# Optimization experiments

Hardware: AMD Instinct MI355X
Metric: run time of the kernel (lower is better)

Reference implementation:

```python
import jax, jax.numpy as jnp
import numpy as np

N = 50000      # nodes
E = 800000     # edges (avg degree 16)
S = 2          # sample_size
D_IN = 128     # input_dim
D_NOISE = 64   # noise_dim
D0 = 256       # output_dims[0]
D1 = 256       # output_dims[1]


def setup_inputs() -> dict:
    key = jax.random.key(0)
    ks = jax.random.split(key, 8)
    X = jax.random.normal(ks[0], (1, N, D_IN), dtype=jnp.float32)
    edge_src = jax.random.randint(ks[1], (E,), 0, N)
    edge_dst = jax.random.randint(ks[2], (E,), 0, N)
    # Bernoulli(0.5) noise, as in torch.distributions.Bernoulli
    epsilon = (jax.random.uniform(ks[3], (S, N, D_NOISE)) < 0.5).astype(jnp.float32)
    W0 = jax.random.normal(ks[4], (D_IN + D_NOISE, D0), dtype=jnp.float32) * 0.05
    b0 = jnp.zeros((D0,), jnp.float32)
    W1 = jax.random.normal(ks[5], (D0, D1), dtype=jnp.float32) * 0.05
    b1 = jnp.zeros((D1,), jnp.float32)
    eps0 = jnp.zeros((), jnp.float32)  # GINConv learnable eps, init 0
    eps1 = jnp.zeros((), jnp.float32)
    return dict(X=X, epsilon=epsilon, edge_src=edge_src, edge_dst=edge_dst,
                W0=W0, b0=b0, W1=W1, b1=b1, eps0=eps0, eps1=eps1)


def reference(X, epsilon, edge_src, edge_dst, W0, b0, W1, b1, eps0, eps1):
    # Expand features over sample dim and concat noise: [S, N, D_IN + D_NOISE]
    feat = jnp.broadcast_to(X, (epsilon.shape[0], X.shape[1], X.shape[2]))
    h = jnp.concatenate([feat, epsilon], axis=2)

    def gin_layer(h, eps, W, b):
        # sum aggregation over in-edges: agg[:, d] += h[:, s] for each edge (s, d)
        agg = jnp.zeros_like(h).at[:, edge_dst, :].add(h[:, edge_src, :])
        return jax.nn.relu(((1.0 + eps) * h + agg) @ W + b)

    h = gin_layer(h, eps0, W0, b0)
    h = gin_layer(h, eps1, W1, b1)
    out = jax.nn.relu(h)  # outer activation applied once more in forward()
    return out, epsilon
```

## Files before the change

### kernel.cpp

```cpp
#include <hip/hip_runtime.h>
#include <hip/hip_bf16.h>

#define NN 50000
#define NE 800000
#define NS 2
#define DIN 128
#define DNOISE 64
#define DH0 192
#define DOUT 256
#define NB 49

typedef __bf16 bf16x8 __attribute__((ext_vector_type(8)));
typedef float floatx4 __attribute__((ext_vector_type(4)));


__device__ inline float bflo(unsigned int u) { return __uint_as_float(u << 16); }
__device__ inline float bfhi(unsigned int u) { return __uint_as_float(u & 0xffff0000u); }
__device__ inline unsigned short f2bf_bits(float x) {
    __hip_bfloat16 b = __float2bfloat16(x);
    return *reinterpret_cast<unsigned short*>(&b);
}
__device__ inline unsigned int pack2(float lo, float hi) {
    return (unsigned int)f2bf_bits(lo) | ((unsigned int)f2bf_bits(hi) << 16);
}


__global__ void count_kernel(const int* __restrict__ dst, int* __restrict__ cnt) {
    int i = blockIdx.x * blockDim.x + threadIdx.x;
    if (i < NE) atomicAdd(&cnt[dst[i]], 1);
}

__global__ __launch_bounds__(1024) void scanA_kernel(const int* __restrict__ cnt, int* __restrict__ bsum) {
    int i = blockIdx.x * 1024 + threadIdx.x;
    int v = (i < NN) ? cnt[i] : 0;
    for (int off = 32; off > 0; off >>= 1) v += __shfl_down(v, off);
    __shared__ int wsum[16];
    if ((threadIdx.x & 63) == 0) wsum[threadIdx.x >> 6] = v;
    __syncthreads();
    if (threadIdx.x == 0) {
        int s = 0;
        for (int k = 0; k < 16; ++k) s += wsum[k];
        bsum[blockIdx.x] = s;
    }
}

__global__ __launch_bounds__(64) void scanB_kernel(int* __restrict__ bsum) {
    int lane = threadIdx.x;
    int orig = (lane < NB) ? bsum[lane] : 0;
    int v = orig;
    for (int off = 1; off < 64; off <<= 1) {
        int t = __shfl_up(v, off);
        if (lane >= off) v += t;
    }
    if (lane < NB) bsum[lane] = v - orig;
}

__global__ __launch_bounds__(1024) void scanC_kernel(int* __restrict__ cnt, const int* __restrict__ bsum,
                                                     int* __restrict__ row_ptr) {
    __shared__ int buf[1024];
    int tid = threadIdx.x;
    int i = blockIdx.x * 1024 + tid;
    int v = (i < NN) ? cnt[i] : 0;
    buf[tid] = v;
    __syncthreads();
    for (int off = 1; off < 1024; off <<= 1) {
        int t = (tid >= off) ? buf[tid - off] : 0;
        __syncthreads();
        buf[tid] += t;
        __syncthreads();
    }
    int excl = buf[tid] - v + bsum[blockIdx.x];
    if (i < NN) { row_ptr[i + 1] = excl + v; cnt[i] = excl; }
    if (i == 0) row_ptr[0] = 0;
}

__global__ void fill_kernel(const int* __restrict__ src, const int* __restrict__ dst,
                            int* __restrict__ cursor, int* __restrict__ col_idx) {
    int i = blockIdx.x * blockDim.x + threadIdx.x;
    if (i < NE) {
        int p = atomicAdd(&cursor[dst[i]], 1);
        col_idx[p] = src[i];
    }
}

#define XQ (NN * DIN / 4)
#define XB4 ((XQ + 255) / 256)
#define NR_BLOCKS ((NS * NN + 255) / 256)

__global__ void prep_kernel(const float* __restrict__ X, unsigned short* __restrict__ Xb,
                            const float* __restrict__ noise, uint2* __restrict__ Nbit,
                            float* __restrict__ out_eps) {
    int b = blockIdx.x;
    if (b < XB4) {
        int i = b * 256 + threadIdx.x;
        if (i < XQ) {
            float4 v = reinterpret_cast<const float4*>(X)[i];
            ushort4 o;
            o.x = f2bf_bits(v.x); o.y = f2bf_bits(v.y); o.z = f2bf_bits(v.z); o.w = f2bf_bits(v.w);
            reinterpret_cast<ushort4*>(Xb)[i] = o;
        }
    } else {
        int r = (b - XB4) * 256 + threadIdx.x;
        if (r < NS * NN) {
            const float4* p = reinterpret_cast<const float4*>(noise + (size_t)r * DNOISE);
            float4* oe = reinterpret_cast<float4*>(out_eps + (size_t)r * DNOISE);
            unsigned int lo = 0, hi = 0;
            for (int q = 0; q < 8; ++q) {
                float4 v = p[q];
                oe[q] = v;
                int base = q * 4;
                lo |= (v.x != 0.f ? 1u : 0u) << base;
                lo |= (v.y != 0.f ? 1u : 0u) << (base + 1);
                lo |= (v.z != 0.f ? 1u : 0u) << (base + 2);
                lo |= (v.w != 0.f ? 1u : 0u) << (base + 3);
            }
            for (int q = 8; q < 16; ++q) {
                float4 v = p[q];
                oe[q] = v;
                int base = q * 4 - 32;
                hi |= (v.x != 0.f ? 1u : 0u) << base;
                hi |= (v.y != 0.f ? 1u : 0u) << (base + 1);
                hi |= (v.z != 0.f ? 1u : 0u) << (base + 2);
                hi |= (v.w != 0.f ? 1u : 0u) << (base + 3);
            }
            uint2 o; o.x = lo; o.y = hi;
            Nbit[r] = o;
        }
    }
}


__global__ void transpose_both(const float* __restrict__ W0, const float* __restrict__ W1,
                               __hip_bfloat16* __restrict__ Wt0, __hip_bfloat16* __restrict__ Wt1) {
    int b = blockIdx.x;
    if (b < DOUT) {
        for (int k = threadIdx.x; k < DH0; k += blockDim.x)
            Wt0[(size_t)b * DH0 + k] = __float2bfloat16(W0[(size_t)k * DOUT + b]);
    } else {
        int n = b - DOUT;
        for (int k = threadIdx.x; k < DOUT; k += blockDim.x)
            Wt1[(size_t)n * DOUT + k] = __float2bfloat16(W1[(size_t)k * DOUT + n]);
    }
}


__global__ __launch_bounds__(256) void agg0_kernel(
    const unsigned int* __restrict__ Xb,
    const uint2* __restrict__ Nbit,
    const int* __restrict__ row_ptr, const int* __restrict__ col_idx,
    const float* __restrict__ eps0p,
    unsigned int* __restrict__ z0) {
    const int d = blockIdx.x * 2 + (threadIdx.x >> 7);
    const int cc = threadIdx.x & 127;
    const float c = 1.f + eps0p[0];
    const int beg = row_ptr[d], end = row_ptr[d + 1];
    if (cc < 64) {
        const unsigned int* src = Xb + cc;
        unsigned int u = src[(size_t)d * 64];
        float aL = c * bflo(u), aH = c * bfhi(u);
        int e = beg;
        for (; e + 3 < end; e += 4) {
            int i0 = col_idx[e], i1 = col_idx[e + 1], i2 = col_idx[e + 2], i3 = col_idx[e + 3];
            unsigned int u0 = src[(size_t)i0 * 64], u1 = src[(size_t)i1 * 64];
            unsigned int u2 = src[(size_t)i2 * 64], u3 = src[(size_t)i3 * 64];
            aL += (bflo(u0) + bflo(u1)) + (bflo(u2) + bflo(u3));
            aH += (bfhi(u0) + bfhi(u1)) + (bfhi(u2) + bfhi(u3));
        }
        for (; e < end; ++e) {
            unsigned int ue = src[(size_t)col_idx[e] * 64];
            aL += bflo(ue); aH += bfhi(ue);
        }
        unsigned int r = pack2(aL, aH);
        z0[(size_t)d * 96 + cc] = r;
        z0[(size_t)(NN + d) * 96 + cc] = r;
    } else {
        int j = cc - 64;
        int s = j >> 5, col = j & 31;
        const uint2* src = Nbit + (size_t)s * NN;
        const int word = col >> 4;
        const int sh = (2 * col) & 31;
        uint2 uS = src[d];
        unsigned int wS = word ? uS.y : uS.x;
        int c0 = 0, c1 = 0;
        int e = beg;
        for (; e + 3 < end; e += 4) {
            uint2 u0 = src[col_idx[e]], u1 = src[col_idx[e + 1]];
            uint2 u2 = src[col_idx[e + 2]], u3 = src[col_idx[e + 3]];
            unsigned int w0 = word ? u0.y : u0.x, w1 = word ? u1.y : u1.x;
            unsigned int w2 = word ? u2.y : u2.x, w3 = word ? u3.y : u3.x;
            c0 += (int)((w0 >> sh) & 1) + (int)((w1 >> sh) & 1) + (int)((w2 >> sh) & 1) + (int)((w3 >> sh) & 1);
            c1 += (int)((w0 >> (sh + 1)) & 1) + (int)((w1 >> (sh + 1)) & 1) +
                  (int)((w2 >> (sh + 1)) & 1) + (int)((w3 >> (sh + 1)) & 1);
        }
        for (; e < end; ++e) {
            uint2 ue = src[col_idx[e]];
            unsigned int we = word ? ue.y : ue.x;
            c0 += (int)((we >> sh) & 1);
            c1 += (int)((we >> (sh + 1)) & 1);
        }
        float aL = c * (float)((wS >> sh) & 1) + (float)c0;
        float aH = c * (float)((wS >> (sh + 1)) & 1) + (float)c1;
        z0[(size_t)(s * NN + d) * 96 + 64 + col] = pack2(aL, aH);
    }
}


__global__ __launch_bounds__(128) void agg1_kernel(
    const uint2* __restrict__ h,
    const int* __restrict__ row_ptr, const int* __restrict__ col_idx,
    const float* __restrict__ eps1p,
    uint2* __restrict__ z1,
    int s) {
    const int d = blockIdx.x * 2 + (threadIdx.x >> 6);
    const int cc = threadIdx.x & 63;
    const float c = 1.f + eps1p[0];
    const int beg = row_ptr[d], end = row_ptr[d + 1];
    const uint2* src = h + (size_t)s * NN * 64 + cc;
    uint2 u = src[(size_t)d * 64];
    float aL0 = c * bflo(u.x), aH0 = c * bfhi(u.x);
    float aL1 = c * bflo(u.y), aH1 = c * bfhi(u.y);
    int e = beg;
    for (; e + 7 < end; e += 8) {
        uint2 g[8];
#pragma unroll
        for (int q = 0; q < 8; ++q) g[q] = src[(size_t)col_idx[e + q] * 64];
#pragma unroll
        for (int q = 0; q < 8; ++q) {
            aL0 += bflo(g[q].x); aH0 += bfhi(g[q].x);
            aL1 += bflo(g[q].y); aH1 += bfhi(g[q].y);
        }
    }
    for (; e + 3 < end; e += 4) {
        uint2 u0 = src[(size_t)col_idx[e] * 64], u1 = src[(size_t)col_idx[e + 1] * 64];
        uint2 u2 = src[(size_t)col_idx[e + 2] * 64], u3 = src[(size_t)col_idx[e + 3] * 64];
        aL0 += (bflo(u0.x) + bflo(u1.x)) + (bflo(u2.x) + bflo(u3.x));
        aH0 += (bfhi(u0.x) + bfhi(u1.x)) + (bfhi(u2.x) + bfhi(u3.x));
        aL1 += (bflo(u0.y) + bflo(u1.y)) + (bflo(u2.y) + bflo(u3.y));
        aH1 += (bfhi(u0.y) + bfhi(u1.y)) + (bfhi(u2.y) + bfhi(u3.y));
    }
    for (; e < end; ++e) {
        uint2 ue = src[(size_t)col_idx[e] * 64];
        aL0 += bflo(ue.x); aH0 += bfhi(ue.x);
        aL1 += bflo(ue.y); aH1 += bfhi(ue.y);
    }
    uint2 r; r.x = pack2(aL0, aH0); r.y = pack2(aL1, aH1);
    z1[(size_t)(s * NN + d) * 64 + cc] = r;
}


__device__ inline void store_out(float* C, size_t idx, float v) { C[idx] = v; }
__device__ inline void store_out(__hip_bfloat16* C, size_t idx, float v) { C[idx] = __float2bfloat16(v); }

template <typename OUT_T>
__global__ __launch_bounds__(256) void gemm_bias_relu(
    const __hip_bfloat16* __restrict__ A, const __hip_bfloat16* __restrict__ Wt,
    const float* __restrict__ bias, OUT_T* __restrict__ C,
    int M, int K) {
    const int lane = threadIdx.x & 63;
    const int wave = threadIdx.x >> 6;
    const int rowBase = blockIdx.x * 128 + wave * 32;
    if (rowBase >= M) return;
    const int lo = lane & 15;
    const int quad = lane >> 4;

    floatx4 acc0[16], acc1[16];
#pragma unroll
    for (int t = 0; t < 16; ++t) {
        acc0[t] = (floatx4){0.f, 0.f, 0.f, 0.f};
        acc1[t] = (floatx4){0.f, 0.f, 0.f, 0.f};
    }

    const __hip_bfloat16* arow0 = A + (size_t)(rowBase + lo) * K + quad * 8;
    const __hip_bfloat16* arow1 = arow0 + (size_t)16 * K;
    for (int k0 = 0; k0 < K; k0 += 32) {
        bf16x8 a0 = *reinterpret_cast<const bf16x8*>(arow0 + k0);
        bf16x8 a1 = *reinterpret_cast<const bf16x8*>(arow1 + k0);
#pragma unroll
        for (int t = 0; t < 16; ++t) {
            bf16x8 b = *reinterpret_cast<const bf16x8*>(Wt + (size_t)(t * 16 + lo) * K + k0 + quad * 8);
            acc0[t] = __builtin_amdgcn_mfma_f32_16x16x32_bf16(a0, b, acc0[t], 0, 0, 0);
            acc1[t] = __builtin_amdgcn_mfma_f32_16x16x32_bf16(a1, b, acc1[t], 0, 0, 0);
        }
    }

#pragma unroll
    for (int t = 0; t < 16; ++t) {
        int col = t * 16 + lo;
        float bv = bias[col];
#pragma unroll
        for (int r = 0; r < 4; ++r) {
            int row0 = rowBase + quad * 4 + r;
            float v0 = acc0[t][r] + bv;
            store_out(C, (size_t)row0 * DOUT + col, v0 > 0.f ? v0 : 0.f);
            float v1 = acc1[t][r] + bv;
            store_out(C, (size_t)(row0 + 16) * DOUT + col, v1 > 0.f ? v1 : 0.f);
        }
    }
}

extern "C" void kernel_launch(void* const* d_in, const int* in_sizes, int n_in,
                              void* d_out, int out_size, void* d_ws, size_t ws_size,
                              hipStream_t stream) {
    const float* X = (const float*)d_in[0];
    const float* noise = (const float*)d_in[1];
    const int* esrc = (const int*)d_in[2];
    const int* edst = (const int*)d_in[3];
    const float* W0 = (const float*)d_in[4];
    const float* b0 = (const float*)d_in[5];
    const float* W1 = (const float*)d_in[6];
    const float* b1 = (const float*)d_in[7];
    const float* eps0 = (const float*)d_in[8];
    const float* eps1 = (const float*)d_in[9];
    float* out = (float*)d_out;

    const int M = NS * NN;

    char* w = (char*)d_ws;
    auto carve = [&](size_t bytes) { char* p = w; w += (bytes + 511) & ~(size_t)511; return p; };
    int* cursor = (int*)carve((size_t)NN * 4);
    int* row_ptr = (int*)carve((size_t)(NN + 1) * 4);
    int* col_idx = (int*)carve((size_t)NE * 4);
    int* bsum = (int*)carve((size_t)NB * 4);
    uint2* Nbit = (uint2*)carve((size_t)M * 8);
    __hip_bfloat16* Wt0 = (__hip_bfloat16*)carve((size_t)DH0 * DOUT * 2);
    __hip_bfloat16* Wt1 = (__hip_bfloat16*)carve((size_t)DOUT * DOUT * 2);
    unsigned int* z = (unsigned int*)carve((size_t)M * DOUT * 2);

    __hip_bfloat16* h1 = (__hip_bfloat16*)d_out;
    unsigned short* Xb = (unsigned short*)(z + (size_t)M * 96);

    hipMemsetAsync(cursor, 0, (size_t)NN * 4, stream);
    count_kernel<<<(NE + 255) / 256, 256, 0, stream>>>(edst, cursor);
    scanA_kernel<<<NB, 1024, 0, stream>>>(cursor, bsum);
    scanB_kernel<<<1, 64, 0, stream>>>(bsum);
    scanC_kernel<<<NB, 1024, 0, stream>>>(cursor, bsum, row_ptr);
    fill_kernel<<<(NE + 255) / 256, 256, 0, stream>>>(esrc, edst, cursor, col_idx);
    prep_kernel<<<XB4 + NR_BLOCKS, 256, 0, stream>>>(X, Xb, noise, Nbit,
                                                     out + (size_t)M * DOUT);
    transpose_both<<<2 * DOUT, 256, 0, stream>>>(W0, W1, Wt0, Wt1);

    agg0_kernel<<<NN / 2, 256, 0, stream>>>(
        (const unsigned int*)Xb, Nbit, row_ptr, col_idx, eps0, z);
    gemm_bias_relu<__hip_bfloat16><<<(M + 127) / 128, 256, 0, stream>>>(
        (const __hip_bfloat16*)z, Wt0, b0, h1, M, DH0);
    agg1_kernel<<<NN / 2, 128, 0, stream>>>(
        (const uint2*)h1, row_ptr, col_idx, eps1, (uint2*)z, 0);
    agg1_kernel<<<NN / 2, 128, 0, stream>>>(
        (const uint2*)h1, row_ptr, col_idx, eps1, (uint2*)z, 1);
    gemm_bias_relu<float><<<(M + 127) / 128, 256, 0, stream>>>(
        (const __hip_bfloat16*)z, Wt1, b1, out, M, DOUT);
}
```

Before: 633.7 us.

## Retile GEMM with LDS-staged swizzled weights and merge per-sample aggregation launches

The GEMM moves from 128-row blocks that each read all 256 output columns of weights straight from global memory to 256x64 tiles. Weight slices are staged in swizzled LDS with a one-step register prefetch, and a grouped block order shares the A rows across the four column groups. The layer-1 aggregation now handles both samples in one 256-thread launch instead of two separate launches. The aim is to cut redundant global weight loads and launch overhead, at the cost of extra barriers and A rows being re-read by four column blocks.

```diff
diff --git a/kernel.cpp b/kernel.cpp
--- a/kernel.cpp
+++ b/kernel.cpp
@@ -205,13 +205,13 @@
 }
 
 
-__global__ __launch_bounds__(128) void agg1_kernel(
+__global__ __launch_bounds__(256) void agg1_kernel(
     const uint2* __restrict__ h,
     const int* __restrict__ row_ptr, const int* __restrict__ col_idx,
     const float* __restrict__ eps1p,
-    uint2* __restrict__ z1,
-    int s) {
-    const int d = blockIdx.x * 2 + (threadIdx.x >> 6);
+    uint2* __restrict__ z1) {
+    const int d = blockIdx.x * 2 + (threadIdx.x >> 7);
+    const int s = (threadIdx.x >> 6) & 1;
     const int cc = threadIdx.x & 63;
     const float c = 1.f + eps1p[0];
     const int beg = row_ptr[d], end = row_ptr[d + 1];
@@ -251,52 +251,110 @@
 __device__ inline void store_out(float* C, size_t idx, float v) { C[idx] = v; }
 __device__ inline void store_out(__hip_bfloat16* C, size_t idx, float v) { C[idx] = __float2bfloat16(v); }
 
-template <typename OUT_T>
+template <int K, typename OUT_T>
 __global__ __launch_bounds__(256) void gemm_bias_relu(
     const __hip_bfloat16* __restrict__ A, const __hip_bfloat16* __restrict__ Wt,
-    const float* __restrict__ bias, OUT_T* __restrict__ C,
-    int M, int K) {
-    const int lane = threadIdx.x & 63;
-    const int wave = threadIdx.x >> 6;
-    const int rowBase = blockIdx.x * 128 + wave * 32;
-    if (rowBase >= M) return;
-    const int lo = lane & 15;
-    const int quad = lane >> 4;
-
-    floatx4 acc0[16], acc1[16];
-#pragma unroll
-    for (int t = 0; t < 16; ++t) {
-        acc0[t] = (floatx4){0.f, 0.f, 0.f, 0.f};
-        acc1[t] = (floatx4){0.f, 0.f, 0.f, 0.f};
-    }
-
-    const __hip_bfloat16* arow0 = A + (size_t)(rowBase + lo) * K + quad * 8;
-    const __hip_bfloat16* arow1 = arow0 + (size_t)16 * K;
-    for (int k0 = 0; k0 < K; k0 += 32) {
-        bf16x8 a0 = *reinterpret_cast<const bf16x8*>(arow0 + k0);
-        bf16x8 a1 = *reinterpret_cast<const bf16x8*>(arow1 + k0);
-#pragma unroll
-        for (int t = 0; t < 16; ++t) {
-            bf16x8 b = *reinterpret_cast<const bf16x8*>(Wt + (size_t)(t * 16 + lo) * K + k0 + quad * 8);
-            acc0[t] = __builtin_amdgcn_mfma_f32_16x16x32_bf16(a0, b, acc0[t], 0, 0, 0);
-            acc1[t] = __builtin_amdgcn_mfma_f32_16x16x32_bf16(a1, b, acc1[t], 0, 0, 0);
-        }
-    }
-
-#pragma unroll
-    for (int t = 0; t < 16; ++t) {
-        int col = t * 16 + lo;
-        float bv = bias[col];
-#pragma unroll
-        for (int r = 0; r < 4; ++r) {
-            int row0 = rowBase + quad * 4 + r;
-            float v0 = acc0[t][r] + bv;
-            store_out(C, (size_t)row0 * DOUT + col, v0 > 0.f ? v0 : 0.f);
-            float v1 = acc1[t][r] + bv;
-            store_out(C, (size_t)(row0 + 16) * DOUT + col, v1 > 0.f ? v1 : 0.f);
-        }
-    }
-}
+    const float* __restrict__ bias, OUT_T* __restrict__ C, int M) {
+    __shared__ uint4 ldsbuf[512];
+    char* lds = (char*)ldsbuf;
+
+    const int p = blockIdx.x;
+    const int mm = p >> 3, rr8 = p & 7;
+    const int cg = mm & 3, qq = mm >> 2;
+    const int rg = qq * 8 + rr8;
+    const int blockRow = rg * 256;
+    if (blockRow >= M) return;
+    const int colBase = cg * 64;
+
+    const int tid = threadIdx.x;
+    const int lane = tid & 63;
+    const int wave = tid >> 6;
+    const int lo = lane & 15, quad = lane >> 4;
+    const int rowBase = blockRow + wave * 64;
+
+    const int n0 = tid >> 3, j0 = tid & 7;
+    const int n1 = n0 + 32;
+    const __hip_bfloat16* wg0 = Wt + (size_t)(colBase + n0) * K + j0 * 8;
+    const __hip_bfloat16* wg1 = Wt + (size_t)(colBase + n1) * K + j0 * 8;
+    const int lw0 = n0 * 128 + ((j0 ^ (n0 & 7)) << 4);
+    const int lw1 = n1 * 128 + ((j0 ^ (n1 & 7)) << 4);
+
+    floatx4 acc[4][4];
+#pragma unroll
+    for (int i = 0; i < 4; ++i)
+#pragma unroll
+        for (int j = 0; j < 4; ++j) acc[i][j] = (floatx4){0.f, 0.f, 0.f, 0.f};
+
+    unsigned int aoff[4];
+#pragma unroll
+    for (int rt = 0; rt < 4; ++rt) {
+        int rowi = rowBase + rt * 16 + lo;
+        if (rowi >= M) rowi = M - 1;
+        aoff[rt] = (unsigned int)rowi * (unsigned int)(K * 2);
+    }
+    const char* Ab = (const char*)A + quad * 16;
+
+    const int NC = K >> 6;
+
+    {
+        uint4 s0 = *(const uint4*)wg0;
+        uint4 s1 = *(const uint4*)wg1;
+        *(uint4*)(lds + lw0) = s0;
+        *(uint4*)(lds + lw1) = s1;
+    }
+    __syncthreads();
+
+    for (int c = 0; c < NC; ++c) {
+        uint4 q0 = {0, 0, 0, 0}, q1 = {0, 0, 0, 0};
+        if (c + 1 < NC) {
+            q0 = *(const uint4*)(wg0 + (c + 1) * 64);
+            q1 = *(const uint4*)(wg1 + (c + 1) * 64);
+        }
+#pragma unroll
+        for (int ks = 0; ks < 2; ++ks) {
+            bf16x8 a[4], b[4];
+            const int kbyte = c * 128 + ks * 64;
+#pragma unroll
+            for (int rt = 0; rt < 4; ++rt)
+                a[rt] = *(const bf16x8*)(Ab + aoff[rt] + kbyte);
+#pragma unroll
+            for (int ct = 0; ct < 4; ++ct) {
+                int nr = ct * 16 + lo;
+                b[ct] = *(const bf16x8*)(lds + nr * 128 + ((((ks << 2) + quad) ^ (nr & 7)) << 4));
+            }
+#pragma unroll
+            for (int rt = 0; rt < 4; ++rt)
+#pragma unroll
+                for (int ct = 0; ct < 4; ++ct)
+                    acc[rt][ct] = __builtin_amdgcn_mfma_f32_16x16x32_bf16(a[rt], b[ct], acc[rt][ct], 0, 0, 0);
+        }
+        __syncthreads();
+        if (c + 1 < NC) {
+            *(uint4*)(lds + lw0) = q0;
+            *(uint4*)(lds + lw1) = q1;
+            __syncthreads();
+        }
+    }
+
+#pragma unroll
+    for (int ct = 0; ct < 4; ++ct) {
+        const int col = colBase + ct * 16 + lo;
+        const float bv = bias[col];
+#pragma unroll
+        for (int rt = 0; rt < 4; ++rt) {
+#pragma unroll
+            for (int r = 0; r < 4; ++r) {
+                int row = rowBase + rt * 16 + quad * 4 + r;
+                if (row < M) {
+                    float v = acc[rt][ct][r] + bv;
+                    store_out(C, (size_t)row * DOUT + col, v > 0.f ? v : 0.f);
+                }
+            }
+        }
+    }
+}
+
+#define GEMM_GRID 1568
 
 extern "C" void kernel_launch(void* const* d_in, const int* in_sizes, int n_in,
                               void* d_out, int out_size, void* d_ws, size_t ws_size,
@@ -341,12 +399,10 @@
 
     agg0_kernel<<<NN / 2, 256, 0, stream>>>(
         (const unsigned int*)Xb, Nbit, row_ptr, col_idx, eps0, z);
-    gemm_bias_relu<__hip_bfloat16><<<(M + 127) / 128, 256, 0, stream>>>(
-        (const __hip_bfloat16*)z, Wt0, b0, h1, M, DH0);
-    agg1_kernel<<<NN / 2, 128, 0, stream>>>(
-        (const uint2*)h1, row_ptr, col_idx, eps1, (uint2*)z, 0);
-    agg1_kernel<<<NN / 2, 128, 0, stream>>>(
-        (const uint2*)h1, row_ptr, col_idx, eps1, (uint2*)z, 1);
-    gemm_bias_relu<float><<<(M + 127) / 128, 256, 0, stream>>>(
-        (const __hip_bfloat16*)z, Wt1, b1, out, M, DOUT);
-}
+    gemm_bias_relu<DH0, __hip_bfloat16><<<GEMM_GRID, 256, 0, stream>>>(
+        (const __hip_bfloat16*)z, Wt0, b0, h1, M);
+    agg1_kernel<<<NN / 2, 256, 0, stream>>>(
+        (const uint2*)h1, row_ptr, col_idx, eps1, (uint2*)z);
+    gemm_bias_relu<DOUT, float><<<GEMM_GRID, 256, 0, stream>>>(
+        (const __hip_bfloat16*)z, Wt1, b1, out, M);
+}
```

Result: faster. 614.5 us (-3.0%).
